# Kernel optimization log

Hardware: AMD Instinct MI355X
Metric: run time of the kernel (lower is better)

## Reference

```python
import jax, jax.numpy as jnp
import numpy as np

T, D, I, E, K = 2048, 2048, 5632, 8, 2


def setup_inputs() -> dict:
    key = jax.random.key(0)
    k1, k2, k3, k4, k5 = jax.random.split(key, 5)
    s = 0.02
    return {
        "x": jax.random.normal(k1, (T, D), dtype=jnp.float32),
        "gate_w": jax.random.normal(k2, (E, D), dtype=jnp.float32) * s,
        "w_gate": jax.random.normal(k3, (E, I, D), dtype=jnp.float32) * s,
        "w_up": jax.random.normal(k4, (E, I, D), dtype=jnp.float32) * s,
        "w_down": jax.random.normal(k5, (E, D, I), dtype=jnp.float32) * s,
    }


def reference(x, gate_w, w_gate, w_up, w_down):
    # Router: logits [T, E], top-k then softmax over the k selected logits
    logits = x @ gate_w.T
    top_vals, top_idx = jax.lax.top_k(logits, K)          # [T, K]
    rw = jax.nn.softmax(top_vals, axis=-1)                # [T, K]
    # Dense combine weights [T, E]: sum of routing weights over selected slots.
    # Mathematically identical to the per-(expert, slot) scatter-add in torch,
    # since duplicate selections of the same expert just sum their weights.
    combine = jnp.sum(jax.nn.one_hot(top_idx, E, dtype=x.dtype) * rw[..., None], axis=1)  # [T, E]
    # SwiGLU expert MLPs, batched over experts (grouped GEMM as dense einsum)
    g = jnp.einsum("td,eid->tei", x, w_gate)              # [T, E, I]
    u = jnp.einsum("td,eid->tei", x, w_up)                # [T, E, I]
    h = jax.nn.silu(g) * u                                 # [T, E, I]
    out_e = jnp.einsum("tei,edi->ted", h, w_down)         # [T, E, D]
    return jnp.einsum("ted,te->td", out_e, combine)       # [T, D]
```

## Files before the change

kernel.cpp:

```cpp
#include <hip/hip_runtime.h>
#include <hip/hip_bf16.h>
#include <stdint.h>

#define TTOK 2048
#define DDIM 2048
#define IDIM 5632
#define NEXP 8

typedef __attribute__((ext_vector_type(8))) short bf16x8;
typedef __attribute__((ext_vector_type(4))) float f32x4;
typedef __attribute__((ext_vector_type(8))) unsigned short u16x8;
typedef __attribute__((ext_vector_type(4))) unsigned short u16x4;

__device__ __forceinline__ unsigned short f2bf(float f) {
  union { float f; uint32_t u; } v; v.f = f;
  uint32_t u = v.u + 0x7fffu + ((v.u >> 16) & 1u);
  return (unsigned short)(u >> 16);
}

__device__ __forceinline__ uint32_t fbits(float f) {
  union { float f; uint32_t u; } v; v.f = f; return v.u;
}

__device__ __forceinline__ u16x8 cvt8t(float4 a, float4 b) {
  union { u16x8 v; uint32_t w[4]; } r;
  r.w[0] = __builtin_amdgcn_perm(fbits(a.y), fbits(a.x), 0x07060302);
  r.w[1] = __builtin_amdgcn_perm(fbits(a.w), fbits(a.z), 0x07060302);
  r.w[2] = __builtin_amdgcn_perm(fbits(b.y), fbits(b.x), 0x07060302);
  r.w[3] = __builtin_amdgcn_perm(fbits(b.w), fbits(b.z), 0x07060302);
  return r.v;
}

typedef __attribute__((address_space(3))) void lds_t;
typedef const __attribute__((address_space(1))) void gbl_t;
__device__ __forceinline__ void gload16(const void* g, void* l) {
  __builtin_amdgcn_global_load_lds((gbl_t*)g, (lds_t*)l, 16, 0, 0);
}

#define GU_BAR() asm volatile("s_waitcnt vmcnt(4) lgkmcnt(0)\n\ts_barrier" ::: "memory")
#define DN_BAR() asm volatile("s_waitcnt vmcnt(0) lgkmcnt(0)\n\ts_barrier" ::: "memory")

__global__ __launch_bounds__(256) void router_kernel(
    const float* __restrict__ x, const float* __restrict__ gw,
    unsigned short* __restrict__ xbf,
    int* __restrict__ cnt, int* __restrict__ slots, float* __restrict__ wts)
{
  const int lane = threadIdx.x & 63;
  const int t = (blockIdx.x * blockDim.x + threadIdx.x) >> 6;
  const float* xr = x + (size_t)t * DDIM;
  float acc[NEXP];
#pragma unroll
  for (int e = 0; e < NEXP; ++e) acc[e] = 0.f;
#pragma unroll
  for (int it = 0; it < DDIM / 256; ++it) {
    const int d = (it * 64 + lane) * 4;
    const float4 xv = *(const float4*)(xr + d);
    u16x4 xb; xb[0]=f2bf(xv.x); xb[1]=f2bf(xv.y); xb[2]=f2bf(xv.z); xb[3]=f2bf(xv.w);
    *(u16x4*)(xbf + (size_t)t * DDIM + d) = xb;
#pragma unroll
    for (int e = 0; e < NEXP; ++e) {
      const float4 gv = *(const float4*)(gw + (size_t)e * DDIM + d);
      acc[e] += xv.x*gv.x + xv.y*gv.y + xv.z*gv.z + xv.w*gv.w;
    }
  }
#pragma unroll
  for (int e = 0; e < NEXP; ++e) {
    float v = acc[e];
#pragma unroll
    for (int off = 32; off > 0; off >>= 1) v += __shfl_xor(v, off);
    acc[e] = v;
  }
  if (lane == 0) {
    int i0 = 0; float v0 = acc[0];
#pragma unroll
    for (int e = 1; e < NEXP; ++e) if (acc[e] > v0) { v0 = acc[e]; i0 = e; }
    int i1 = -1; float v1 = -3.4e38f;
#pragma unroll
    for (int e = 0; e < NEXP; ++e) { if (e == i0) continue; if (acc[e] > v1) { v1 = acc[e]; i1 = e; } }
    const float e1 = __expf(v1 - v0);
    const float w0 = 1.f / (1.f + e1);
    const float w1 = e1 / (1.f + e1);
    const int p0 = atomicAdd(&cnt[i0], 1);
    slots[i0 * TTOK + p0] = t * 2;     wts[i0 * TTOK + p0] = w0;
    const int p1 = atomicAdd(&cnt[i1], 1);
    slots[i1 * TTOK + p1] = t * 2 + 1; wts[i1 * TTOK + p1] = w1;
  }
}

__global__ void plan_kernel(const int* __restrict__ cnt,
                            int* __restrict__ tilemap, int* __restrict__ ntiles)
{
  if (threadIdx.x == 0 && blockIdx.x == 0) {
    int n = 0;
#pragma unroll
    for (int e = 0; e < NEXP; ++e) {
      const int nt = (cnt[e] + 127) >> 7;
      for (int m = 0; m < nt; ++m) tilemap[n++] = (e << 8) | m;
    }
    ntiles[0] = n;
  }
}


__global__ __launch_bounds__(256, 3) void gateup_kernel(
    const unsigned short* __restrict__ xbf,
    const float* __restrict__ wg, const float* __restrict__ wu,
    const int* __restrict__ cnt, const int* __restrict__ slots,
    const int* __restrict__ tilemap, const int* __restrict__ ntiles,
    unsigned short* __restrict__ h)
{
  const int flat = (blockIdx.x & 7) * 440 + (blockIdx.x >> 3);
  const int ti = flat % 40;
  if (ti >= ntiles[0]) return;
  const int em = tilemap[ti];
  const int e = em >> 8;
  const int mt = em & 255;
  const int n0 = (flat / 40) * 64;
  const int count = cnt[e];
  const int m0 = mt * 128;

  __shared__ unsigned short A[2][128][32];
  __shared__ unsigned short Bg[2][64][32];
  __shared__ unsigned short Bu[2][64][32];
  __shared__ int rslot[128];
  __shared__ int rtok[128];

  const int tid = threadIdx.x;
  const int lane = tid & 63;
  const int wid = tid >> 6;

  if (tid < 128) {
    const int idx = m0 + tid;
    const int safe = slots[e * TTOK + m0];
    const int s = (idx < count) ? slots[e * TTOK + idx] : safe;
    rslot[tid] = (idx < count) ? s : -1;
    rtok[tid] = s >> 1;
  }
  __syncthreads();

  const unsigned short* aptr[2];
#pragma unroll
  for (int j = 0; j < 2; ++j) {
    const int arow = wid * 32 + j * 16 + (lane >> 2);
    aptr[j] = xbf + (size_t)rtok[arow] * DDIM + (((lane & 3) ^ (arow & 3)) * 8);
  }

  const int brow = tid >> 2;
  const int lc = tid & 3;
  const int bslot = lc ^ (brow & 3);
  const size_t wo = (size_t)e * IDIM * DDIM + (size_t)(n0 + brow) * DDIM + lc * 8;
  const float* gsrc = wg + wo;
  const float* usrc = wu + wo;

  const int wr = wid >> 1, wc = wid & 1;
  const int fr = lane & 15;
  const int kc = lane >> 4;

  f32x4 accg[4][2] = {};
  f32x4 accu[4][2] = {};

  float4 Pg[2], Pu[2];
  gload16(aptr[0], &A[0][wid * 32][0]);
  gload16(aptr[1], &A[0][wid * 32 + 16][0]);
  Pg[0] = *(const float4*)(gsrc);     Pg[1] = *(const float4*)(gsrc + 4);
  Pu[0] = *(const float4*)(usrc);     Pu[1] = *(const float4*)(usrc + 4);
  *(u16x8*)&Bg[0][brow][bslot * 8] = cvt8t(Pg[0], Pg[1]);
  *(u16x8*)&Bu[0][brow][bslot * 8] = cvt8t(Pu[0], Pu[1]);
  Pg[0] = *(const float4*)(gsrc + 32); Pg[1] = *(const float4*)(gsrc + 36);
  Pu[0] = *(const float4*)(usrc + 32); Pu[1] = *(const float4*)(usrc + 36);
  GU_BAR();

#pragma unroll 2
  for (int t = 0; t < 64; ++t) {
    const int cur = t & 1;
    const int kpA = ((t + 1 < 64) ? t + 1 : 63) * 32;
    const int kpB = ((t + 2 < 64) ? t + 2 : 63) * 32;

    gload16(aptr[0] + kpA, &A[cur ^ 1][wid * 32][0]);
    gload16(aptr[1] + kpA, &A[cur ^ 1][wid * 32 + 16][0]);
    __builtin_amdgcn_sched_barrier(0);
    *(u16x8*)&Bg[cur ^ 1][brow][bslot * 8] = cvt8t(Pg[0], Pg[1]);
    *(u16x8*)&Bu[cur ^ 1][brow][bslot * 8] = cvt8t(Pu[0], Pu[1]);
    Pg[0] = *(const float4*)(gsrc + kpB);     Pg[1] = *(const float4*)(gsrc + kpB + 4);
    Pu[0] = *(const float4*)(usrc + kpB);     Pu[1] = *(const float4*)(usrc + kpB + 4);
    __builtin_amdgcn_sched_barrier(0);

    __builtin_amdgcn_s_setprio(1);
    bf16x8 a[4], bg[2], bu[2];
#pragma unroll
    for (int mf = 0; mf < 4; ++mf) {
      const int r = wr * 64 + mf * 16 + fr;
      a[mf] = *(const bf16x8*)&A[cur][r][(kc ^ (r & 3)) * 8];
    }
#pragma unroll
    for (int nf = 0; nf < 2; ++nf) {
      const int rb = wc * 32 + nf * 16 + fr;
      bg[nf] = *(const bf16x8*)&Bg[cur][rb][(kc ^ (rb & 3)) * 8];
      bu[nf] = *(const bf16x8*)&Bu[cur][rb][(kc ^ (rb & 3)) * 8];
    }
#pragma unroll
    for (int mf = 0; mf < 4; ++mf)
#pragma unroll
      for (int nf = 0; nf < 2; ++nf) {
        accg[mf][nf] = __builtin_amdgcn_mfma_f32_16x16x32_bf16(a[mf], bg[nf], accg[mf][nf], 0, 0, 0);
        accu[mf][nf] = __builtin_amdgcn_mfma_f32_16x16x32_bf16(a[mf], bu[nf], accu[mf][nf], 0, 0, 0);
      }
    __builtin_amdgcn_s_setprio(0);

    GU_BAR();
  }

#pragma unroll
  for (int mf = 0; mf < 4; ++mf)
#pragma unroll
    for (int nf = 0; nf < 2; ++nf)
#pragma unroll
      for (int j = 0; j < 4; ++j) {
        const int r = wr * 64 + mf * 16 + (lane >> 4) * 4 + j;
        const int s = rslot[r];
        if (s >= 0) {
          const float g = accg[mf][nf][j];
          const float u = accu[mf][nf][j];
          const float hv = g / (1.f + __expf(-g)) * u;
          h[(size_t)s * IDIM + n0 + wc * 32 + nf * 16 + fr] = f2bf(hv);
        }
      }
}

__global__ __launch_bounds__(256, 4) void down_kernel(
    const unsigned short* __restrict__ h,
    const float* __restrict__ wd,
    const int* __restrict__ cnt, const int* __restrict__ slots,
    const float* __restrict__ wts,
    const int* __restrict__ tilemap, const int* __restrict__ ntiles,
    float* __restrict__ out)
{
  const int flat = (blockIdx.x & 7) * 320 + (blockIdx.x >> 3);
  const int ti = flat % 40;
  if (ti >= ntiles[0]) return;
  const int em = tilemap[ti];
  const int e = em >> 8;
  const int mt = em & 255;
  const int rest = flat / 40;
  const int n0 = (rest & 31) * 64;
  const int kbase = (rest >> 5) * (IDIM / 2);
  const int count = cnt[e];
  const int m0 = mt * 128;

  __shared__ unsigned short A[2][128][32];
  __shared__ float Bf[2][64][32];
  __shared__ int rslot[128];
  __shared__ float rw[128];

  const int tid = threadIdx.x;
  const int lane = tid & 63;
  const int wid = tid >> 6;

  if (tid < 128) {
    const int idx = m0 + tid;
    const int safe = slots[e * TTOK + m0];
    const int s = (idx < count) ? slots[e * TTOK + idx] : safe;
    rslot[tid] = (idx < count) ? s : (safe | 0x40000000);
    rw[tid] = (idx < count) ? wts[e * TTOK + idx] : 0.f;
  }
  __syncthreads();

  const unsigned short* aptr[2];
#pragma unroll
  for (int j = 0; j < 2; ++j) {
    const int arow = wid * 32 + j * 16 + (lane >> 2);
    aptr[j] = h + (size_t)(rslot[arow] & 0x3fffffff) * IDIM + kbase
              + (((lane & 3) ^ (arow & 3)) * 8);
  }

  const float* bptr[2];
#pragma unroll
  for (int j = 0; j < 2; ++j) {
    const int browg = wid * 16 + j * 8 + (lane >> 3);
    bptr[j] = wd + (size_t)e * DDIM * IDIM + (size_t)(n0 + browg) * IDIM + kbase
              + (((lane & 7) ^ (browg & 7)) * 4);
  }

  const int wr = wid >> 1, wc = wid & 1;
  const int fr = lane & 15;
  const int kc = lane >> 4;

  f32x4 acc[4][2] = {};

  gload16(aptr[0], &A[0][wid * 32][0]);
  gload16(aptr[1], &A[0][wid * 32 + 16][0]);
  gload16(bptr[0], &Bf[0][wid * 16][0]);
  gload16(bptr[1], &Bf[0][wid * 16 + 8][0]);
  DN_BAR();

#pragma unroll 2
  for (int t = 0; t < 88; ++t) {
    const int cur = t & 1;
    if (t < 87) {
      const int kp = (t + 1) * 32;
      gload16(aptr[0] + kp, &A[cur ^ 1][wid * 32][0]);
      gload16(aptr[1] + kp, &A[cur ^ 1][wid * 32 + 16][0]);
      gload16(bptr[0] + kp, &Bf[cur ^ 1][wid * 16][0]);
      gload16(bptr[1] + kp, &Bf[cur ^ 1][wid * 16 + 8][0]);
    }
    __builtin_amdgcn_sched_barrier(0);

    __builtin_amdgcn_s_setprio(1);
    bf16x8 a[4], b[2];
#pragma unroll
    for (int mf = 0; mf < 4; ++mf) {
      const int r = wr * 64 + mf * 16 + fr;
      a[mf] = *(const bf16x8*)&A[cur][r][(kc ^ (r & 3)) * 8];
    }
#pragma unroll
    for (int nf = 0; nf < 2; ++nf) {
      const int rb = wc * 32 + nf * 16 + fr;
      const int c0 = kc * 2;
      const float4 fa = *(const float4*)&Bf[cur][rb][((c0)     ^ (rb & 7)) * 4];
      const float4 fb = *(const float4*)&Bf[cur][rb][((c0 + 1) ^ (rb & 7)) * 4];
      b[nf] = (bf16x8)cvt8t(fa, fb);
    }
#pragma unroll
    for (int mf = 0; mf < 4; ++mf)
#pragma unroll
      for (int nf = 0; nf < 2; ++nf)
        acc[mf][nf] = __builtin_amdgcn_mfma_f32_16x16x32_bf16(a[mf], b[nf], acc[mf][nf], 0, 0, 0);
    __builtin_amdgcn_s_setprio(0);

    DN_BAR();
  }

#pragma unroll
  for (int mf = 0; mf < 4; ++mf)
#pragma unroll
    for (int j = 0; j < 4; ++j) {
      const int r = wr * 64 + mf * 16 + (lane >> 4) * 4 + j;
      const int s = rslot[r];
      if (!(s & 0x40000000)) {
        const int t2 = s >> 1;
        const float w = rw[r];
#pragma unroll
        for (int nf = 0; nf < 2; ++nf)
          atomicAdd(out + (size_t)t2 * DDIM + n0 + wc * 32 + nf * 16 + fr,
                    acc[mf][nf][j] * w);
      }
    }
}

extern "C" void kernel_launch(void* const* d_in, const int* in_sizes, int n_in,
                              void* d_out, int out_size, void* d_ws, size_t ws_size,
                              hipStream_t stream) {
  const float* x  = (const float*)d_in[0];
  const float* gw = (const float*)d_in[1];
  const float* wg = (const float*)d_in[2];
  const float* wu = (const float*)d_in[3];
  const float* wd = (const float*)d_in[4];
  float* out = (float*)d_out;

  char* ws = (char*)d_ws;
  unsigned short* xbf = (unsigned short*)ws;
  unsigned short* h   = (unsigned short*)(ws + 8388608);
  int*   slots = (int*)(ws + 8388608 + 46137344);
  float* wts   = (float*)(ws + 8388608 + 46137344 + 65536);
  int*   cnt   = (int*)(ws + 8388608 + 46137344 + 131072);
  int*   tmap  = (int*)(ws + 8388608 + 46137344 + 131072 + 32);
  int*   ntl   = (int*)(ws + 8388608 + 46137344 + 131072 + 288);

  hipMemsetAsync(cnt, 0, NEXP * sizeof(int), stream);
  hipMemsetAsync(d_out, 0, (size_t)TTOK * DDIM * sizeof(float), stream);

  router_kernel<<<TTOK / 4, 256, 0, stream>>>(x, gw, xbf, cnt, slots, wts);
  plan_kernel<<<1, 64, 0, stream>>>(cnt, tmap, ntl);
  gateup_kernel<<<3520, 256, 0, stream>>>(xbf, wg, wu, cnt, slots, tmap, ntl, h);
  down_kernel<<<2560, 256, 0, stream>>>(h, wd, cnt, slots, wts, tmap, ntl, out);
}
```

Measured before the change: 791.8 us.

## Widen expert GEMM N-tiles to 128 and convert down-proj weights to bf16 on staging

Result: slower. 847.3 us (+7.0%).

```diff
diff --git a/kernel.cpp b/kernel.cpp
--- a/kernel.cpp
+++ b/kernel.cpp
@@ -37,8 +37,8 @@
   __builtin_amdgcn_global_load_lds((gbl_t*)g, (lds_t*)l, 16, 0, 0);
 }
 
-#define GU_BAR() asm volatile("s_waitcnt vmcnt(4) lgkmcnt(0)\n\ts_barrier" ::: "memory")
-#define DN_BAR() asm volatile("s_waitcnt vmcnt(0) lgkmcnt(0)\n\ts_barrier" ::: "memory")
+#define GU_BAR() asm volatile("s_waitcnt vmcnt(8) lgkmcnt(0)\n\ts_barrier" ::: "memory")
+#define DN_BAR() asm volatile("s_waitcnt vmcnt(4) lgkmcnt(0)\n\ts_barrier" ::: "memory")
 
 __global__ __launch_bounds__(256) void router_kernel(
     const float* __restrict__ x, const float* __restrict__ gw,
@@ -102,26 +102,26 @@
 }
 
 
-__global__ __launch_bounds__(256, 3) void gateup_kernel(
+__global__ __launch_bounds__(256, 2) void gateup_kernel(
     const unsigned short* __restrict__ xbf,
     const float* __restrict__ wg, const float* __restrict__ wu,
     const int* __restrict__ cnt, const int* __restrict__ slots,
     const int* __restrict__ tilemap, const int* __restrict__ ntiles,
     unsigned short* __restrict__ h)
 {
-  const int flat = (blockIdx.x & 7) * 440 + (blockIdx.x >> 3);
+  const int flat = (blockIdx.x & 7) * 220 + (blockIdx.x >> 3);
   const int ti = flat % 40;
   if (ti >= ntiles[0]) return;
   const int em = tilemap[ti];
   const int e = em >> 8;
   const int mt = em & 255;
-  const int n0 = (flat / 40) * 64;
+  const int n0 = (flat / 40) * 128;
   const int count = cnt[e];
   const int m0 = mt * 128;
 
   __shared__ unsigned short A[2][128][32];
-  __shared__ unsigned short Bg[2][64][32];
-  __shared__ unsigned short Bu[2][64][32];
+  __shared__ unsigned short Bg[2][128][32];
+  __shared__ unsigned short Bu[2][128][32];
   __shared__ int rslot[128];
   __shared__ int rtok[128];
 
@@ -142,32 +142,37 @@
 #pragma unroll
   for (int j = 0; j < 2; ++j) {
     const int arow = wid * 32 + j * 16 + (lane >> 2);
-    aptr[j] = xbf + (size_t)rtok[arow] * DDIM + (((lane & 3) ^ (arow & 3)) * 8);
-  }
-
-  const int brow = tid >> 2;
-  const int lc = tid & 3;
-  const int bslot = lc ^ (brow & 3);
-  const size_t wo = (size_t)e * IDIM * DDIM + (size_t)(n0 + brow) * DDIM + lc * 8;
+    aptr[j] = xbf + (size_t)rtok[arow] * DDIM + (((lane & 3) ^ ((arow >> 2) & 3)) * 8);
+  }
+
+  const int brow = tid >> 1;
+  const int lc0 = (tid & 1) * 2;
+  const int swzb = (brow >> 2) & 3;
+  const int s0 = (lc0 ^ swzb) * 8;
+  const int s1 = ((lc0 + 1) ^ swzb) * 8;
+  const size_t wo = (size_t)e * IDIM * DDIM + (size_t)(n0 + brow) * DDIM + lc0 * 8;
   const float* gsrc = wg + wo;
   const float* usrc = wu + wo;
 
   const int wr = wid >> 1, wc = wid & 1;
   const int fr = lane & 15;
   const int kc = lane >> 4;
-
-  f32x4 accg[4][2] = {};
-  f32x4 accu[4][2] = {};
-
-  float4 Pg[2], Pu[2];
+  const int rsw = (fr >> 2) & 3;
+
+  f32x4 accg[4][4] = {};
+  f32x4 accu[4][4] = {};
+
+  float4 Pg[4], Pu[4];
   gload16(aptr[0], &A[0][wid * 32][0]);
   gload16(aptr[1], &A[0][wid * 32 + 16][0]);
-  Pg[0] = *(const float4*)(gsrc);     Pg[1] = *(const float4*)(gsrc + 4);
-  Pu[0] = *(const float4*)(usrc);     Pu[1] = *(const float4*)(usrc + 4);
-  *(u16x8*)&Bg[0][brow][bslot * 8] = cvt8t(Pg[0], Pg[1]);
-  *(u16x8*)&Bu[0][brow][bslot * 8] = cvt8t(Pu[0], Pu[1]);
-  Pg[0] = *(const float4*)(gsrc + 32); Pg[1] = *(const float4*)(gsrc + 36);
-  Pu[0] = *(const float4*)(usrc + 32); Pu[1] = *(const float4*)(usrc + 36);
+#pragma unroll
+  for (int q = 0; q < 4; ++q) { Pg[q] = *(const float4*)(gsrc + q * 4); Pu[q] = *(const float4*)(usrc + q * 4); }
+  *(u16x8*)&Bg[0][brow][s0] = cvt8t(Pg[0], Pg[1]);
+  *(u16x8*)&Bg[0][brow][s1] = cvt8t(Pg[2], Pg[3]);
+  *(u16x8*)&Bu[0][brow][s0] = cvt8t(Pu[0], Pu[1]);
+  *(u16x8*)&Bu[0][brow][s1] = cvt8t(Pu[2], Pu[3]);
+#pragma unroll
+  for (int q = 0; q < 4; ++q) { Pg[q] = *(const float4*)(gsrc + 32 + q * 4); Pu[q] = *(const float4*)(usrc + 32 + q * 4); }
   GU_BAR();
 
 #pragma unroll 2
@@ -179,29 +184,29 @@
     gload16(aptr[0] + kpA, &A[cur ^ 1][wid * 32][0]);
     gload16(aptr[1] + kpA, &A[cur ^ 1][wid * 32 + 16][0]);
     __builtin_amdgcn_sched_barrier(0);
-    *(u16x8*)&Bg[cur ^ 1][brow][bslot * 8] = cvt8t(Pg[0], Pg[1]);
-    *(u16x8*)&Bu[cur ^ 1][brow][bslot * 8] = cvt8t(Pu[0], Pu[1]);
-    Pg[0] = *(const float4*)(gsrc + kpB);     Pg[1] = *(const float4*)(gsrc + kpB + 4);
-    Pu[0] = *(const float4*)(usrc + kpB);     Pu[1] = *(const float4*)(usrc + kpB + 4);
+    *(u16x8*)&Bg[cur ^ 1][brow][s0] = cvt8t(Pg[0], Pg[1]);
+    *(u16x8*)&Bg[cur ^ 1][brow][s1] = cvt8t(Pg[2], Pg[3]);
+    *(u16x8*)&Bu[cur ^ 1][brow][s0] = cvt8t(Pu[0], Pu[1]);
+    *(u16x8*)&Bu[cur ^ 1][brow][s1] = cvt8t(Pu[2], Pu[3]);
+#pragma unroll
+    for (int q = 0; q < 4; ++q) { Pg[q] = *(const float4*)(gsrc + kpB + q * 4); Pu[q] = *(const float4*)(usrc + kpB + q * 4); }
     __builtin_amdgcn_sched_barrier(0);
 
     __builtin_amdgcn_s_setprio(1);
-    bf16x8 a[4], bg[2], bu[2];
-#pragma unroll
-    for (int mf = 0; mf < 4; ++mf) {
-      const int r = wr * 64 + mf * 16 + fr;
-      a[mf] = *(const bf16x8*)&A[cur][r][(kc ^ (r & 3)) * 8];
+    bf16x8 a[4], bg[4], bu[4];
+    const int cs = (kc ^ rsw) * 8;
+#pragma unroll
+    for (int mf = 0; mf < 4; ++mf)
+      a[mf] = *(const bf16x8*)&A[cur][wr * 64 + mf * 16 + fr][cs];
+#pragma unroll
+    for (int nf = 0; nf < 4; ++nf) {
+      bg[nf] = *(const bf16x8*)&Bg[cur][wc * 64 + nf * 16 + fr][cs];
+      bu[nf] = *(const bf16x8*)&Bu[cur][wc * 64 + nf * 16 + fr][cs];
     }
 #pragma unroll
-    for (int nf = 0; nf < 2; ++nf) {
-      const int rb = wc * 32 + nf * 16 + fr;
-      bg[nf] = *(const bf16x8*)&Bg[cur][rb][(kc ^ (rb & 3)) * 8];
-      bu[nf] = *(const bf16x8*)&Bu[cur][rb][(kc ^ (rb & 3)) * 8];
-    }
-#pragma unroll
     for (int mf = 0; mf < 4; ++mf)
 #pragma unroll
-      for (int nf = 0; nf < 2; ++nf) {
+      for (int nf = 0; nf < 4; ++nf) {
         accg[mf][nf] = __builtin_amdgcn_mfma_f32_16x16x32_bf16(a[mf], bg[nf], accg[mf][nf], 0, 0, 0);
         accu[mf][nf] = __builtin_amdgcn_mfma_f32_16x16x32_bf16(a[mf], bu[nf], accu[mf][nf], 0, 0, 0);
       }
@@ -213,7 +218,7 @@
 #pragma unroll
   for (int mf = 0; mf < 4; ++mf)
 #pragma unroll
-    for (int nf = 0; nf < 2; ++nf)
+    for (int nf = 0; nf < 4; ++nf)
 #pragma unroll
       for (int j = 0; j < 4; ++j) {
         const int r = wr * 64 + mf * 16 + (lane >> 4) * 4 + j;
@@ -222,12 +227,12 @@
           const float g = accg[mf][nf][j];
           const float u = accu[mf][nf][j];
           const float hv = g / (1.f + __expf(-g)) * u;
-          h[(size_t)s * IDIM + n0 + wc * 32 + nf * 16 + fr] = f2bf(hv);
+          h[(size_t)s * IDIM + n0 + wc * 64 + nf * 16 + fr] = f2bf(hv);
         }
       }
 }
 
-__global__ __launch_bounds__(256, 4) void down_kernel(
+__global__ __launch_bounds__(256, 3) void down_kernel(
     const unsigned short* __restrict__ h,
     const float* __restrict__ wd,
     const int* __restrict__ cnt, const int* __restrict__ slots,
@@ -235,20 +240,20 @@
     const int* __restrict__ tilemap, const int* __restrict__ ntiles,
     float* __restrict__ out)
 {
-  const int flat = (blockIdx.x & 7) * 320 + (blockIdx.x >> 3);
+  const int flat = (blockIdx.x & 7) * 160 + (blockIdx.x >> 3);
   const int ti = flat % 40;
   if (ti >= ntiles[0]) return;
   const int em = tilemap[ti];
   const int e = em >> 8;
   const int mt = em & 255;
   const int rest = flat / 40;
-  const int n0 = (rest & 31) * 64;
-  const int kbase = (rest >> 5) * (IDIM / 2);
+  const int n0 = (rest & 15) * 128;
+  const int kbase = (rest >> 4) * (IDIM / 2);
   const int count = cnt[e];
   const int m0 = mt * 128;
 
   __shared__ unsigned short A[2][128][32];
-  __shared__ float Bf[2][64][32];
+  __shared__ unsigned short B[2][128][32];
   __shared__ int rslot[128];
   __shared__ float rw[128];
 
@@ -270,60 +275,62 @@
   for (int j = 0; j < 2; ++j) {
     const int arow = wid * 32 + j * 16 + (lane >> 2);
     aptr[j] = h + (size_t)(rslot[arow] & 0x3fffffff) * IDIM + kbase
-              + (((lane & 3) ^ (arow & 3)) * 8);
-  }
-
-  const float* bptr[2];
-#pragma unroll
-  for (int j = 0; j < 2; ++j) {
-    const int browg = wid * 16 + j * 8 + (lane >> 3);
-    bptr[j] = wd + (size_t)e * DDIM * IDIM + (size_t)(n0 + browg) * IDIM + kbase
-              + (((lane & 7) ^ (browg & 7)) * 4);
-  }
+              + (((lane & 3) ^ ((arow >> 2) & 3)) * 8);
+  }
+
+  const int brow = tid >> 1;
+  const int lc0 = (tid & 1) * 2;
+  const int swzb = (brow >> 2) & 3;
+  const int s0 = (lc0 ^ swzb) * 8;
+  const int s1 = ((lc0 + 1) ^ swzb) * 8;
+  const float* bsrc = wd + (size_t)e * DDIM * IDIM + (size_t)(n0 + brow) * IDIM + kbase + lc0 * 8;
 
   const int wr = wid >> 1, wc = wid & 1;
   const int fr = lane & 15;
   const int kc = lane >> 4;
-
-  f32x4 acc[4][2] = {};
-
+  const int rsw = (fr >> 2) & 3;
+
+  f32x4 acc[4][4] = {};
+
+  float4 P[4];
   gload16(aptr[0], &A[0][wid * 32][0]);
   gload16(aptr[1], &A[0][wid * 32 + 16][0]);
-  gload16(bptr[0], &Bf[0][wid * 16][0]);
-  gload16(bptr[1], &Bf[0][wid * 16 + 8][0]);
+#pragma unroll
+  for (int q = 0; q < 4; ++q) P[q] = *(const float4*)(bsrc + q * 4);
+  *(u16x8*)&B[0][brow][s0] = cvt8t(P[0], P[1]);
+  *(u16x8*)&B[0][brow][s1] = cvt8t(P[2], P[3]);
+#pragma unroll
+  for (int q = 0; q < 4; ++q) P[q] = *(const float4*)(bsrc + 32 + q * 4);
   DN_BAR();
 
 #pragma unroll 2
   for (int t = 0; t < 88; ++t) {
     const int cur = t & 1;
-    if (t < 87) {
-      const int kp = (t + 1) * 32;
-      gload16(aptr[0] + kp, &A[cur ^ 1][wid * 32][0]);
-      gload16(aptr[1] + kp, &A[cur ^ 1][wid * 32 + 16][0]);
-      gload16(bptr[0] + kp, &Bf[cur ^ 1][wid * 16][0]);
-      gload16(bptr[1] + kp, &Bf[cur ^ 1][wid * 16 + 8][0]);
-    }
+    const int kpA = ((t + 1 < 88) ? t + 1 : 87) * 32;
+    const int kpB = ((t + 2 < 88) ? t + 2 : 87) * 32;
+
+    gload16(aptr[0] + kpA, &A[cur ^ 1][wid * 32][0]);
+    gload16(aptr[1] + kpA, &A[cur ^ 1][wid * 32 + 16][0]);
     __builtin_amdgcn_sched_barrier(0);
+    *(u16x8*)&B[cur ^ 1][brow][s0] = cvt8t(P[0], P[1]);
+    *(u16x8*)&B[cur ^ 1][brow][s1] = cvt8t(P[2], P[3]);
+#pragma unroll
+    for (int q = 0; q < 4; ++q) P[q] = *(const float4*)(bsrc + kpB + q * 4);
+    __builtin_amdgcn_sched_barrier(0);
 
     __builtin_amdgcn_s_setprio(1);
-    bf16x8 a[4], b[2];
-#pragma unroll
-    for (int mf = 0; mf < 4; ++mf) {
-      const int r = wr * 64 + mf * 16 + fr;
-      a[mf] = *(const bf16x8*)&A[cur][r][(kc ^ (r & 3)) * 8];
-    }
-#pragma unroll
-    for (int nf = 0; nf < 2; ++nf) {
-      const int rb = wc * 32 + nf * 16 + fr;
-      const int c0 = kc * 2;
-      const float4 fa = *(const float4*)&Bf[cur][rb][((c0)     ^ (rb & 7)) * 4];
-      const float4 fb = *(const float4*)&Bf[cur][rb][((c0 + 1) ^ (rb & 7)) * 4];
-      b[nf] = (bf16x8)cvt8t(fa, fb);
-    }
+    bf16x8 a[4], b[4];
+    const int cs = (kc ^ rsw) * 8;
 #pragma unroll
     for (int mf = 0; mf < 4; ++mf)
-#pragma unroll
-      for (int nf = 0; nf < 2; ++nf)
+      a[mf] = *(const bf16x8*)&A[cur][wr * 64 + mf * 16 + fr][cs];
+#pragma unroll
+    for (int nf = 0; nf < 4; ++nf)
+      b[nf] = *(const bf16x8*)&B[cur][wc * 64 + nf * 16 + fr][cs];
+#pragma unroll
+    for (int mf = 0; mf < 4; ++mf)
+#pragma unroll
+      for (int nf = 0; nf < 4; ++nf)
         acc[mf][nf] = __builtin_amdgcn_mfma_f32_16x16x32_bf16(a[mf], b[nf], acc[mf][nf], 0, 0, 0);
     __builtin_amdgcn_s_setprio(0);
 
@@ -340,8 +347,8 @@
         const int t2 = s >> 1;
         const float w = rw[r];
 #pragma unroll
-        for (int nf = 0; nf < 2; ++nf)
-          atomicAdd(out + (size_t)t2 * DDIM + n0 + wc * 32 + nf * 16 + fr,
+        for (int nf = 0; nf < 4; ++nf)
+          atomicAdd(out + (size_t)t2 * DDIM + n0 + wc * 64 + nf * 16 + fr,
                     acc[mf][nf][j] * w);
       }
     }
@@ -371,6 +378,6 @@
 
   router_kernel<<<TTOK / 4, 256, 0, stream>>>(x, gw, xbf, cnt, slots, wts);
   plan_kernel<<<1, 64, 0, stream>>>(cnt, tmap, ntl);
-  gateup_kernel<<<3520, 256, 0, stream>>>(xbf, wg, wu, cnt, slots, tmap, ntl, h);
-  down_kernel<<<2560, 256, 0, stream>>>(h, wd, cnt, slots, wts, tmap, ntl, out);
-}
+  gateup_kernel<<<1760, 256, 0, stream>>>(xbf, wg, wu, cnt, slots, tmap, ntl, h);
+  down_kernel<<<1280, 256, 0, stream>>>(h, wd, cnt, slots, wts, tmap, ntl, out);
+}
```
